# Kernel optimization log

Measured on AMD Instinct MI355X. Metric: run time of the kernel, lower is better.

Reference implementation:

```python
import jax, jax.numpy as jnp
import numpy as np

N = 100000  # num nodes


def _gcn_conv(x, src, dst, W, b, n_nodes):
    """PyG GCNConv: symmetric normalization with implicit self-loops.
    out = D^{-1/2} (A + I) D^{-1/2} (x W) + b, deg counts in-edges + self-loop.
    """
    h = x @ W  # [N, H]
    ones = jnp.ones(src.shape[0], dtype=x.dtype)
    deg = jax.ops.segment_sum(ones, dst, num_segments=n_nodes) + 1.0  # +1 self-loop
    dinv = jax.lax.rsqrt(deg)  # [N]
    norm = dinv[src] * dinv[dst]  # [E]
    msg = h[src] * norm[:, None]  # gather + scale: memory-bound
    agg = jax.ops.segment_sum(msg, dst, num_segments=n_nodes)
    agg = agg + h * (dinv * dinv)[:, None]  # self-loop contribution
    return agg + b


def setup_inputs() -> dict:
    key = jax.random.key(0)
    k1, k2, k3, k4 = jax.random.split(key, 4)
    F = 64
    E = 1600000
    x = jax.random.normal(k1, (N, F), dtype=jnp.float32)
    edge_index = jax.random.randint(k2, (2, E), 0, N, dtype=jnp.int64)
    W1 = jax.random.normal(k3, (F, F), dtype=jnp.float32) / jnp.sqrt(jnp.float32(F))
    b1 = jnp.zeros((F,), dtype=jnp.float32)
    W2 = jax.random.normal(k4, (F, F), dtype=jnp.float32) / jnp.sqrt(jnp.float32(F))
    b2 = jnp.zeros((F,), dtype=jnp.float32)
    return {"x": x, "edge_index": edge_index, "W1": W1, "b1": b1, "W2": W2, "b2": b2}


def reference(x, edge_index, W1, b1, W2, b2):
    src, dst = edge_index[0], edge_index[1]
    h = _gcn_conv(x, src, dst, W1, b1, N)
    h = jax.nn.relu(h)
    # dropout(p=0.1) is identity in eval mode
    h = _gcn_conv(h, src, dst, W2, b2, N)
    return jax.nn.relu(h)
```

## Files before the change

### kernel.cpp

```cpp
#include <hip/hip_runtime.h>
#include <hip/hip_bf16.h>
#include <stdint.h>

#define NN 100000
#define NE 1600000
#define NBLK 256
#define EPB (NE / NBLK)
#define NBINS 782
#define NCELL (NBINS * NBLK)
#define NSB ((NCELL + 1023) / 1024)


__device__ __forceinline__ unsigned pack_bf16(float a, float b) {
    unsigned ua = __float_as_uint(a);
    unsigned ub = __float_as_uint(b);
    ua += 0x7FFFu + ((ua >> 16) & 1u);
    ub += 0x7FFFu + ((ub >> 16) & 1u);
    return (ua >> 16) | (ub & 0xFFFF0000u);
}
#define BF_LO(w) __uint_as_float((w) << 16)
#define BF_HI(w) __uint_as_float((w) & 0xFFFF0000u)


__global__ void k_detect(const int* __restrict__ ei, int* __restrict__ flag) {
    if (threadIdx.x == 0) {
        int z = 0;
#pragma unroll
        for (int i = 0; i < 16; ++i) z |= ei[2 * i + 1];
        flag[0] = (z == 0) ? 1 : 0;
    }
}


__global__ void __launch_bounds__(256) k_hist(const int* __restrict__ ei,
                                              const int* __restrict__ flag,
                                              int* __restrict__ gcount) {
    __shared__ int lbin[NBINS];
    int t = threadIdx.x, blk = blockIdx.x;
    for (int i = t; i < NBINS; i += 256) lbin[i] = 0;
    __syncthreads();
    int is64 = flag[0];
    int e0 = blk * EPB;
    if (is64) {
        const int2* p = (const int2*)ei;
        for (int e = e0 + t; e < e0 + EPB; e += 256)
            atomicAdd(&lbin[p[NE + e].x >> 7], 1);
    } else {
        for (int e = e0 + t; e < e0 + EPB; e += 256)
            atomicAdd(&lbin[ei[NE + e] >> 7], 1);
    }
    __syncthreads();
    for (int b = t; b < NBINS; b += 256) gcount[b * NBLK + blk] = lbin[b];
}

__global__ void k_pscan1(const int* __restrict__ g, int* __restrict__ bsum) {
    __shared__ int sh[256];
    int t = threadIdx.x;
    int base = blockIdx.x * 1024 + t * 4;
    int s = 0;
#pragma unroll
    for (int j = 0; j < 4; ++j) { int i = base + j; if (i < NCELL) s += g[i]; }
    sh[t] = s; __syncthreads();
    for (int off = 128; off > 0; off >>= 1) {
        if (t < off) sh[t] += sh[t + off];
        __syncthreads();
    }
    if (t == 0) bsum[blockIdx.x] = sh[0];
}

__global__ void k_pscan2(const int* __restrict__ bsum, int* __restrict__ boff) {
    __shared__ int sh[256];
    int t = threadIdx.x;
    int v = (t < NSB) ? bsum[t] : 0;
    sh[t] = v; __syncthreads();
    for (int off = 1; off < 256; off <<= 1) {
        int tmp = (t >= off) ? sh[t - off] : 0;
        __syncthreads();
        sh[t] += tmp;
        __syncthreads();
    }
    if (t < NSB) boff[t] = sh[t] - v;
}

__global__ void k_pscan3(const int* __restrict__ g, const int* __restrict__ boff,
                         int* __restrict__ goff) {
    __shared__ int sh[256];
    int t = threadIdx.x;
    int base = blockIdx.x * 1024 + t * 4;
    int v[4]; int s = 0;
#pragma unroll
    for (int j = 0; j < 4; ++j) { int i = base + j; v[j] = (i < NCELL) ? g[i] : 0; s += v[j]; }
    sh[t] = s; __syncthreads();
    for (int off = 1; off < 256; off <<= 1) {
        int tmp = (t >= off) ? sh[t - off] : 0;
        __syncthreads();
        sh[t] += tmp;
        __syncthreads();
    }
    int run = sh[t] - s + boff[blockIdx.x];
#pragma unroll
    for (int j = 0; j < 4; ++j) {
        int i = base + j;
        if (i < NCELL) { goff[i] = run; run += v[j]; }
    }
}

__global__ void __launch_bounds__(256) k_scatter(const int* __restrict__ ei,
                                                 const int* __restrict__ flag,
                                                 const int* __restrict__ goff,
                                                 unsigned* __restrict__ tmp) {
    __shared__ int lcur[NBINS];
    int t = threadIdx.x, blk = blockIdx.x;
    for (int i = t; i < NBINS; i += 256) lcur[i] = 0;
    __syncthreads();
    int is64 = flag[0];
    int e0 = blk * EPB;
    for (int e = e0 + t; e < e0 + EPB; e += 256) {
        int s, d;
        if (is64) {
            s = ((const int2*)ei)[e].x;
            d = ((const int2*)ei)[NE + e].x;
        } else {
            s = ei[e];
            d = ei[NE + e];
        }
        int b = d >> 7;
        int lr = atomicAdd(&lcur[b], 1);
        int pos = goff[b * NBLK + blk] + lr;
        tmp[pos] = (unsigned)s | ((unsigned)(d & 127) << 17);
    }
}

__global__ void __launch_bounds__(256) k_deg(const unsigned* __restrict__ tmp,
                                             const int* __restrict__ goff,
                                             int* __restrict__ rs,
                                             int* __restrict__ deg32,
                                             float* __restrict__ dinv) {
    __shared__ int hist[128];
    int b = blockIdx.x, t = threadIdx.x;
    if (t < 128) hist[t] = 0;
    __syncthreads();
    int bs = goff[b * NBLK];
    int be = (b == NBINS - 1) ? NE : goff[(b + 1) * NBLK];
    for (int e = bs + t; e < be; e += 256)
        atomicAdd(&hist[tmp[e] >> 17], 1);
    __syncthreads();
    if (t < 128) {
        int node = b * 128 + t;
        if (node < NN) {
            int c = hist[t];
            int loff = 0;
            for (int i = 0; i < t; ++i) loff += hist[i];
            rs[node] = bs + loff;
            deg32[node] = c;
            dinv[node] = rsqrtf((float)c + 1.0f);
        }
    }
    if (b == 0 && t == 0) rs[NN] = NE;
}

__global__ void __launch_bounds__(256) k_csr(const unsigned* __restrict__ tmp,
                                             const int* __restrict__ goff,
                                             const int* __restrict__ rs,
                                             const int* __restrict__ deg32,
                                             unsigned* __restrict__ csr) {
    __shared__ int cur[128];
    __shared__ int base_sh[128];
    int b = blockIdx.x, t = threadIdx.x;
    if (t < 128) {
        cur[t] = 0;
        int node = b * 128 + t;
        base_sh[t] = (node < NN) ? rs[node] : 0;
    }
    __syncthreads();
    int bs = goff[b * NBLK];
    int be = (b == NBINS - 1) ? NE : goff[(b + 1) * NBLK];
    for (int e = bs + t; e < be; e += 256) {
        unsigned v = tmp[e];
        int dl = v >> 17;
        unsigned s = v & 0x1FFFFu;
        int lr = atomicAdd(&cur[dl], 1);
        unsigned deg = (unsigned)min(deg32[s], 2047);
        csr[base_sh[dl] + lr] = (s << 3) | (deg << 21);
    }
}


__global__ void __launch_bounds__(256) k_gemm(const float* __restrict__ X,
                                              const float* __restrict__ W,
                                              unsigned* __restrict__ Hb) {
    int wid = (blockIdx.x * 256 + threadIdx.x) >> 6;
    int lane = threadIdx.x & 63;
    int task = __builtin_amdgcn_readfirstlane(wid);
    const int ntasks = ((NN + 63) >> 6) * 2;
    if (task >= ntasks) return;
    int t = task >> 1;
    int ch = task & 1;
    int row = t * 64 + lane;
    int r = row < NN ? row : NN - 1;
    const float4* xp = (const float4*)(X + (size_t)r * 64);
    const float* Wb = W + ch * 32;
    float acc[32];
#pragma unroll
    for (int c = 0; c < 32; ++c) acc[c] = 0.f;
#pragma unroll 4
    for (int k4 = 0; k4 < 16; ++k4) {
        float4 xv = xp[k4];
#pragma unroll
        for (int kj = 0; kj < 4; ++kj) {
            float xk = (kj == 0) ? xv.x : (kj == 1) ? xv.y : (kj == 2) ? xv.z : xv.w;
            const float4* wr = (const float4*)(Wb + (k4 * 4 + kj) * 64);
#pragma unroll
            for (int c4 = 0; c4 < 8; ++c4) {
                float4 wv = wr[c4];
                acc[c4 * 4 + 0] += xk * wv.x;
                acc[c4 * 4 + 1] += xk * wv.y;
                acc[c4 * 4 + 2] += xk * wv.z;
                acc[c4 * 4 + 3] += xk * wv.w;
            }
        }
    }
    uint4* op = (uint4*)(Hb + (size_t)r * 32 + ch * 16);
#pragma unroll
    for (int q = 0; q < 4; ++q) {
        uint4 o;
        o.x = pack_bf16(acc[q * 8 + 0], acc[q * 8 + 1]);
        o.y = pack_bf16(acc[q * 8 + 2], acc[q * 8 + 3]);
        o.z = pack_bf16(acc[q * 8 + 4], acc[q * 8 + 5]);
        o.w = pack_bf16(acc[q * 8 + 6], acc[q * 8 + 7]);
        op[q] = o;
    }
}


#define EDGE_ACC(p, r)                                                        \
    {                                                                         \
        float w = rsqrtf((float)((p) >> 21) + 1.0f);                          \
        a0 += BF_LO((r).x) * w; a1 += BF_HI((r).x) * w;                       \
        a2 += BF_LO((r).y) * w; a3 += BF_HI((r).y) * w;                       \
        a4 += BF_LO((r).z) * w; a5 += BF_HI((r).z) * w;                       \
        a6 += BF_LO((r).w) * w; a7 += BF_HI((r).w) * w;                       \
    }

__global__ void __launch_bounds__(256) k_agg(const uint4* __restrict__ hb,
                                             const int* __restrict__ rs,
                                             const unsigned* __restrict__ csr,
                                             const float* __restrict__ dinv,
                                             const float* __restrict__ bias,
                                             float4* __restrict__ out4) {
    int wid = (blockIdx.x * blockDim.x + threadIdx.x) >> 6;
    int lane = threadIdx.x & 63;
    int node = __builtin_amdgcn_readfirstlane(wid);
    if (node >= NN) return;
    int g = lane >> 3;
    int s = lane & 7;
    float dn = dinv[node];
    int e0 = rs[node], e1 = rs[node + 1];
    float a0 = 0.f, a1 = 0.f, a2 = 0.f, a3 = 0.f;
    float a4 = 0.f, a5 = 0.f, a6 = 0.f, a7 = 0.f;
    int e = e0 + g;
    unsigned p0 = csr[e];
    unsigned p1 = csr[e + 8];
    for (; e + 8 < e1; e += 16) {
        unsigned q0 = csr[e + 16];
        unsigned q1 = csr[e + 24];
        uint4 r0 = hb[(p0 & 0x1FFFFFu) + s];
        uint4 r1 = hb[(p1 & 0x1FFFFFu) + s];
        EDGE_ACC(p0, r0);
        EDGE_ACC(p1, r1);
        p0 = q0; p1 = q1;
    }
    if (e < e1) {
        uint4 r0 = hb[(p0 & 0x1FFFFFu) + s];
        EDGE_ACC(p0, r0);
    }
#pragma unroll
    for (int m = 8; m <= 32; m <<= 1) {
        a0 += __shfl_xor(a0, m); a1 += __shfl_xor(a1, m);
        a2 += __shfl_xor(a2, m); a3 += __shfl_xor(a3, m);
        a4 += __shfl_xor(a4, m); a5 += __shfl_xor(a5, m);
        a6 += __shfl_xor(a6, m); a7 += __shfl_xor(a7, m);
    }
    if (lane < 8) {
        uint4 r = hb[(size_t)node * 8 + s];
        const float4* bp = (const float4*)(bias + s * 8);
        float4 b0 = bp[0], b1v = bp[1];
        float4 o0, o1;
        o0.x = fmaxf((a0 + BF_LO(r.x) * dn) * dn + b0.x, 0.f);
        o0.y = fmaxf((a1 + BF_HI(r.x) * dn) * dn + b0.y, 0.f);
        o0.z = fmaxf((a2 + BF_LO(r.y) * dn) * dn + b0.z, 0.f);
        o0.w = fmaxf((a3 + BF_HI(r.y) * dn) * dn + b0.w, 0.f);
        o1.x = fmaxf((a4 + BF_LO(r.z) * dn) * dn + b1v.x, 0.f);
        o1.y = fmaxf((a5 + BF_HI(r.z) * dn) * dn + b1v.y, 0.f);
        o1.z = fmaxf((a6 + BF_LO(r.w) * dn) * dn + b1v.z, 0.f);
        o1.w = fmaxf((a7 + BF_HI(r.w) * dn) * dn + b1v.w, 0.f);
        out4[(size_t)node * 16 + s * 2] = o0;
        out4[(size_t)node * 16 + s * 2 + 1] = o1;
    }
}


extern "C" void kernel_launch(void* const* d_in, const int* in_sizes, int n_in,
                              void* d_out, int out_size, void* d_ws, size_t ws_size,
                              hipStream_t stream) {
    const float* x  = (const float*)d_in[0];
    const int* ei   = (const int*)d_in[1];
    const float* W1 = (const float*)d_in[2];
    const float* b1 = (const float*)d_in[3];
    const float* W2 = (const float*)d_in[4];
    const float* b2 = (const float*)d_in[5];

    char* ws = (char*)d_ws;
    size_t off = 0;
    auto alloc = [&](size_t bytes) -> char* {
        char* p = ws + off;
        off = (off + bytes + 511) & ~(size_t)511;
        return p;
    };
    int*      flag  = (int*)alloc(64);
    int*      gcount= (int*)alloc((size_t)NCELL * 4);
    int*      goff  = (int*)alloc((size_t)NCELL * 4);
    int*      bsum  = (int*)alloc((size_t)NSB * 4);
    int*      boff  = (int*)alloc((size_t)NSB * 4);
    unsigned* tmp   = (unsigned*)alloc((size_t)NE * 4);
    unsigned* csr   = (unsigned*)alloc((size_t)NE * 4);
    int*      rs    = (int*)alloc((size_t)(NN + 1) * 4);
    int*      deg32 = (int*)alloc((size_t)NN * 4);
    float*    dinv  = (float*)alloc((size_t)NN * 4);
    unsigned* hbuf  = (unsigned*)alloc((size_t)NN * 32 * 4);
    float*    hmid  = (float*)d_out;

    k_detect<<<1, 64, 0, stream>>>(ei, flag);
    k_hist<<<NBLK, 256, 0, stream>>>(ei, flag, gcount);
    k_pscan1<<<NSB, 256, 0, stream>>>(gcount, bsum);
    k_pscan2<<<1, 256, 0, stream>>>(bsum, boff);
    k_pscan3<<<NSB, 256, 0, stream>>>(gcount, boff, goff);
    k_scatter<<<NBLK, 256, 0, stream>>>(ei, flag, goff, tmp);
    k_deg<<<NBINS, 256, 0, stream>>>(tmp, goff, rs, deg32, dinv);
    k_csr<<<NBINS, 256, 0, stream>>>(tmp, goff, rs, deg32, csr);

    k_gemm<<<782, 256, 0, stream>>>(x, W1, hbuf);
    k_agg<<<(NN * 64) / 256, 256, 0, stream>>>((const uint4*)hbuf, rs, csr, dinv, b1,
                                               (float4*)hmid);
    k_gemm<<<782, 256, 0, stream>>>(hmid, W2, hbuf);
    k_agg<<<(NN * 64) / 256, 256, 0, stream>>>((const uint4*)hbuf, rs, csr, dinv, b2,
                                               (float4*)d_out);
}
```

Measured before the change: 270.9 us.

## Fuse first GEMM into histogram launch and quadruple binning block count

The first-layer GEMM is folded into the histogram kernel as extra blocks, so the dense X·W1 work runs alongside edge binning instead of as a separate launch after CSR construction. The number of edge-partition blocks goes from 256 to 1024, with a bounded last chunk, to raise parallelism in the histogram and scatter passes. pscan2 is extended so each thread handles four partial sums, since the block-sum count now exceeds 256. The cost is a larger count/offset table (4x cells) for the scans and more scatter blocks with smaller per-block work.

Measured after the change: 285.4 us. 5.4% more time.

```diff
diff --git a/kernel.cpp b/kernel.cpp
--- a/kernel.cpp
+++ b/kernel.cpp
@@ -4,8 +4,8 @@
 
 #define NN 100000
 #define NE 1600000
-#define NBLK 256
-#define EPB (NE / NBLK)
+#define NBLK 1024
+#define EPB 1563
 #define NBINS 782
 #define NCELL (NBINS * NBLK)
 #define NSB ((NCELL + 1023) / 1024)
@@ -32,26 +32,81 @@
 }
 
 
-__global__ void __launch_bounds__(256) k_hist(const int* __restrict__ ei,
-                                              const int* __restrict__ flag,
-                                              int* __restrict__ gcount) {
+__device__ __forceinline__ void gemm_body(int task, int lane,
+                                          const float* __restrict__ X,
+                                          const float* __restrict__ W,
+                                          unsigned* __restrict__ Hb) {
+    const int ntasks = ((NN + 63) >> 6) * 2;
+    if (task >= ntasks) return;
+    int t = task >> 1;
+    int ch = task & 1;
+    int row = t * 64 + lane;
+    int r = row < NN ? row : NN - 1;
+    const float4* xp = (const float4*)(X + (size_t)r * 64);
+    const float* Wb = W + ch * 32;
+    float acc[32];
+#pragma unroll
+    for (int c = 0; c < 32; ++c) acc[c] = 0.f;
+#pragma unroll 4
+    for (int k4 = 0; k4 < 16; ++k4) {
+        float4 xv = xp[k4];
+#pragma unroll
+        for (int kj = 0; kj < 4; ++kj) {
+            float xk = (kj == 0) ? xv.x : (kj == 1) ? xv.y : (kj == 2) ? xv.z : xv.w;
+            const float4* wr = (const float4*)(Wb + (k4 * 4 + kj) * 64);
+#pragma unroll
+            for (int c4 = 0; c4 < 8; ++c4) {
+                float4 wv = wr[c4];
+                acc[c4 * 4 + 0] += xk * wv.x;
+                acc[c4 * 4 + 1] += xk * wv.y;
+                acc[c4 * 4 + 2] += xk * wv.z;
+                acc[c4 * 4 + 3] += xk * wv.w;
+            }
+        }
+    }
+    uint4* op = (uint4*)(Hb + (size_t)r * 32 + ch * 16);
+#pragma unroll
+    for (int q = 0; q < 4; ++q) {
+        uint4 o;
+        o.x = pack_bf16(acc[q * 8 + 0], acc[q * 8 + 1]);
+        o.y = pack_bf16(acc[q * 8 + 2], acc[q * 8 + 3]);
+        o.z = pack_bf16(acc[q * 8 + 4], acc[q * 8 + 5]);
+        o.w = pack_bf16(acc[q * 8 + 6], acc[q * 8 + 7]);
+        op[q] = o;
+    }
+}
+
+
+__global__ void __launch_bounds__(256) k_hist_gemm(const int* __restrict__ ei,
+                                                   const int* __restrict__ flag,
+                                                   int* __restrict__ gcount,
+                                                   const float* __restrict__ X,
+                                                   const float* __restrict__ W,
+                                                   unsigned* __restrict__ Hb) {
     __shared__ int lbin[NBINS];
+    if (blockIdx.x >= NBLK) {
+        int wid = ((blockIdx.x - NBLK) * 256 + threadIdx.x) >> 6;
+        gemm_body(__builtin_amdgcn_readfirstlane(wid), threadIdx.x & 63, X, W, Hb);
+        return;
+    }
     int t = threadIdx.x, blk = blockIdx.x;
     for (int i = t; i < NBINS; i += 256) lbin[i] = 0;
     __syncthreads();
     int is64 = flag[0];
     int e0 = blk * EPB;
+    int eend = min(e0 + EPB, NE);
     if (is64) {
         const int2* p = (const int2*)ei;
-        for (int e = e0 + t; e < e0 + EPB; e += 256)
+        for (int e = e0 + t; e < eend; e += 256)
             atomicAdd(&lbin[p[NE + e].x >> 7], 1);
     } else {
-        for (int e = e0 + t; e < e0 + EPB; e += 256)
+        for (int e = e0 + t; e < eend; e += 256)
             atomicAdd(&lbin[ei[NE + e] >> 7], 1);
     }
     __syncthreads();
     for (int b = t; b < NBINS; b += 256) gcount[b * NBLK + blk] = lbin[b];
 }
+
 
 __global__ void k_pscan1(const int* __restrict__ g, int* __restrict__ bsum) {
     __shared__ int sh[256];
@@ -71,15 +126,26 @@
 __global__ void k_pscan2(const int* __restrict__ bsum, int* __restrict__ boff) {
     __shared__ int sh[256];
     int t = threadIdx.x;
-    int v = (t < NSB) ? bsum[t] : 0;
-    sh[t] = v; __syncthreads();
+    int v[4]; int s = 0;
+#pragma unroll
+    for (int j = 0; j < 4; ++j) {
+        int i = t * 4 + j;
+        v[j] = (i < NSB) ? bsum[i] : 0;
+        s += v[j];
+    }
+    sh[t] = s; __syncthreads();
     for (int off = 1; off < 256; off <<= 1) {
         int tmp = (t >= off) ? sh[t - off] : 0;
         __syncthreads();
         sh[t] += tmp;
         __syncthreads();
     }
-    if (t < NSB) boff[t] = sh[t] - v;
+    int run = sh[t] - s;
+#pragma unroll
+    for (int j = 0; j < 4; ++j) {
+        int i = t * 4 + j;
+        if (i < NSB) { boff[i] = run; run += v[j]; }
+    }
 }
 
 __global__ void k_pscan3(const int* __restrict__ g, const int* __restrict__ boff,
@@ -115,7 +181,8 @@
     __syncthreads();
     int is64 = flag[0];
     int e0 = blk * EPB;
-    for (int e = e0 + t; e < e0 + EPB; e += 256) {
+    int eend = min(e0 + EPB, NE);
+    for (int e = e0 + t; e < eend; e += 256) {
         int s, d;
         if (is64) {
             s = ((const int2*)ei)[e].x;
@@ -190,46 +257,7 @@
                                               const float* __restrict__ W,
                                               unsigned* __restrict__ Hb) {
     int wid = (blockIdx.x * 256 + threadIdx.x) >> 6;
-    int lane = threadIdx.x & 63;
-    int task = __builtin_amdgcn_readfirstlane(wid);
-    const int ntasks = ((NN + 63) >> 6) * 2;
-    if (task >= ntasks) return;
-    int t = task >> 1;
-    int ch = task & 1;
-    int row = t * 64 + lane;
-    int r = row < NN ? row : NN - 1;
-    const float4* xp = (const float4*)(X + (size_t)r * 64);
-    const float* Wb = W + ch * 32;
-    float acc[32];
-#pragma unroll
-    for (int c = 0; c < 32; ++c) acc[c] = 0.f;
-#pragma unroll 4
-    for (int k4 = 0; k4 < 16; ++k4) {
-        float4 xv = xp[k4];
-#pragma unroll
-        for (int kj = 0; kj < 4; ++kj) {
-            float xk = (kj == 0) ? xv.x : (kj == 1) ? xv.y : (kj == 2) ? xv.z : xv.w;
-            const float4* wr = (const float4*)(Wb + (k4 * 4 + kj) * 64);
-#pragma unroll
-            for (int c4 = 0; c4 < 8; ++c4) {
-                float4 wv = wr[c4];
-                acc[c4 * 4 + 0] += xk * wv.x;
-                acc[c4 * 4 + 1] += xk * wv.y;
-                acc[c4 * 4 + 2] += xk * wv.z;
-                acc[c4 * 4 + 3] += xk * wv.w;
-            }
-        }
-    }
-    uint4* op = (uint4*)(Hb + (size_t)r * 32 + ch * 16);
-#pragma unroll
-    for (int q = 0; q < 4; ++q) {
-        uint4 o;
-        o.x = pack_bf16(acc[q * 8 + 0], acc[q * 8 + 1]);
-        o.y = pack_bf16(acc[q * 8 + 2], acc[q * 8 + 3]);
-        o.z = pack_bf16(acc[q * 8 + 4], acc[q * 8 + 5]);
-        o.w = pack_bf16(acc[q * 8 + 6], acc[q * 8 + 7]);
-        op[q] = o;
-    }
+    gemm_body(__builtin_amdgcn_readfirstlane(wid), threadIdx.x & 63, X, W, Hb);
 }
 
 
@@ -331,7 +359,7 @@
     float*    hmid  = (float*)d_out;
 
     k_detect<<<1, 64, 0, stream>>>(ei, flag);
-    k_hist<<<NBLK, 256, 0, stream>>>(ei, flag, gcount);
+    k_hist_gemm<<<NBLK + 782, 256, 0, stream>>>(ei, flag, gcount, x, W1, hbuf);
     k_pscan1<<<NSB, 256, 0, stream>>>(gcount, bsum);
     k_pscan2<<<1, 256, 0, stream>>>(bsum, boff);
     k_pscan3<<<NSB, 256, 0, stream>>>(gcount, boff, goff);
@@ -339,7 +367,6 @@
     k_deg<<<NBINS, 256, 0, stream>>>(tmp, goff, rs, deg32, dinv);
     k_csr<<<NBINS, 256, 0, stream>>>(tmp, goff, rs, deg32, csr);
 
-    k_gemm<<<782, 256, 0, stream>>>(x, W1, hbuf);
     k_agg<<<(NN * 64) / 256, 256, 0, stream>>>((const uint4*)hbuf, rs, csr, dinv, b1,
                                                (float4*)hmid);
     k_gemm<<<782, 256, 0, stream>>>(hmid, W2, hbuf);
```
